# Performance work log

Measured on AMD Instinct MI355X. Metric: run time of the kernel, lower is better.

Reference implementation:

```python
import jax, jax.numpy as jnp
import numpy as np

B, DIM, H, W = 2, 384, 256, 256
HID = DIM * 1          # ffn_expansion_factor = 1 (required for source code to be consistent)
P = 8                  # patch_size


def setup_inputs() -> dict:
    key = jax.random.key(0)
    k0, k1, k2, k3, k4 = jax.random.split(key, 5)
    x = jax.random.normal(k0, (B, DIM, H, W), jnp.float32)
    # learned spectral filter: (hidden, P, P//2+1), real-valued, multiplies rfft2 coeffs
    fft_filter = jax.random.normal(k1, (HID, P, P // 2 + 1), jnp.float32)
    # project_in: 1x1 conv dim->hidden, weight (out,in)
    w_in = jax.random.normal(k2, (HID, DIM), jnp.float32) * (1.0 / np.sqrt(DIM))
    # depthwise 3x3 conv, groups=channels, weight (C,1,3,3)
    w_dw = jax.random.normal(k3, (HID, 1, 3, 3), jnp.float32) * (1.0 / 3.0)
    # project_out: 1x1 conv hidden//2 -> dim
    w_out = jax.random.normal(k4, (DIM, HID // 2), jnp.float32) * (1.0 / np.sqrt(HID // 2))
    return {"x": x, "fft_filter": fft_filter, "w_in": w_in, "w_dw": w_dw, "w_out": w_out}


def reference(x, fft_filter, w_in, w_dw, w_out):
    b, c, h, w = x.shape
    hid = w_in.shape[0]
    hb, wb = h // P, w // P
    # project_in (1x1 conv == channel GEMM)
    t = jnp.einsum('bchw,oc->bohw', x, w_in)
    # patchify into 8x8 blocks and apply per-patch 2D real FFT spectral filter.
    # reshape b c (hb p1) (wb p2) -> b c hb p1 wb p2; FFT over axes (3,5).
    tp = t.reshape(b, hid, hb, P, wb, P)
    tf = jnp.fft.rfft2(tp, axes=(3, 5))                 # (b,hid,hb,P,wb,P//2+1) complex
    tf = tf * fft_filter[None, :, None, :, None, :]
    tp = jnp.fft.irfft2(tf, s=(P, P), axes=(3, 5))
    t = tp.reshape(b, hid, h, w)
    # depthwise 3x3 conv, stride 1, padding 1
    t = jax.lax.conv_general_dilated(
        t, w_dw, window_strides=(1, 1), padding='SAME',
        feature_group_count=hid,
        dimension_numbers=('NCHW', 'OIHW', 'NCHW'))
    # gated GELU (exact erf gelu, matching torch F.gelu default)
    x1, x2 = t[:, : hid // 2], t[:, hid // 2:]
    g = jax.nn.gelu(x1, approximate=False) * x2
    # project_out (1x1 conv)
    return jnp.einsum('bchw,oc->bohw', g, w_out)
```

## Files before the change

kernel.cpp:

```cpp
#include <hip/hip_runtime.h>
#include <hip/hip_bf16.h>
#include <math.h>

#define BB 2
#define DIM 384
#define HID 384
#define HW 65536

typedef short s16x8 __attribute__((ext_vector_type(8)));
typedef short s16x4 __attribute__((ext_vector_type(4)));
typedef __bf16 bf16x8 __attribute__((ext_vector_type(8)));
typedef float f32x4 __attribute__((ext_vector_type(4)));

__device__ inline short f2b(float f) {
    __hip_bfloat16 h = __float2bfloat16(f);
    return __builtin_bit_cast(short, h);
}
__device__ inline float b2f(short s) {
    return __bfloat162float(__builtin_bit_cast(__hip_bfloat16, s));
}

__device__ inline void gl_lds16(const short* g, short* l) {
    __builtin_amdgcn_global_load_lds(
        (const __attribute__((address_space(1))) unsigned int*)g,
        (__attribute__((address_space(3))) unsigned int*)l, 16, 0, 0);
}

__global__ void k_precompute(const float* __restrict__ F, float* __restrict__ K) {
    int c = blockIdx.x;
    int t = threadIdx.x;
    int a = t >> 3, b = t & 7;
    const float ctab[8] = {1.f, 0.70710678118654752f, 0.f, -0.70710678118654752f,
                           -1.f, -0.70710678118654752f, 0.f, 0.70710678118654752f};
    const float* Fc = F + c * 40;
    float acc = 0.f;
#pragma unroll
    for (int up = 0; up < 8; ++up) {
#pragma unroll
        for (int vp = 0; vp < 5; ++vp) {
            float wv = (vp == 0 || vp == 4) ? 1.f : 2.f;
            int k = (a * up + b * vp) & 7;
            acc += wv * Fc[up * 5 + vp] * ctab[k];
        }
    }
    K[c * 64 + t] = acc * (1.f / 64.f);
}

__global__ void k_cvtw(const float* __restrict__ in, short* __restrict__ out, int n) {
    int i = blockIdx.x * 256 + threadIdx.x;
    if (i < n) out[i] = f2b(in[i]);
}

__global__ __launch_bounds__(256) void k_cvtx(const float* __restrict__ X, short* __restrict__ Xt) {
    int hw0 = blockIdx.x * 64, c0 = blockIdx.y * 64, b = blockIdx.z;
    __shared__ __align__(16) short S[64 * 64];
    int t = threadIdx.x;
    const float* Xb = X + ((size_t)(b * DIM) << 16);
    short* Xtb = Xt + (size_t)b * HW * DIM;
#pragma unroll
    for (int p = 0; p < 2; ++p) {
        int row = p * 32 + (t >> 3), sb = t & 7;
        const float* src = &Xb[((size_t)(c0 + row) << 16) + hw0 + sb * 8];
        float4 a = *(const float4*)src;
        float4 bq = *(const float4*)(src + 4);
        s16x8 v;
        v[0] = f2b(a.x);  v[1] = f2b(a.y);  v[2] = f2b(a.z);  v[3] = f2b(a.w);
        v[4] = f2b(bq.x); v[5] = f2b(bq.y); v[6] = f2b(bq.z); v[7] = f2b(bq.w);
        *(s16x8*)&S[row * 64 + ((sb ^ (row >> 3)) << 3)] = v;
    }
    __syncthreads();
#pragma unroll
    for (int p = 0; p < 2; ++p) {
        int row = p * 32 + (t >> 3), ch = t & 7;
        s16x8 v;
#pragma unroll
        for (int j = 0; j < 8; ++j)
            v[j] = S[(ch * 8 + j) * 64 + (row ^ (ch << 3))];
        *(s16x8*)&Xtb[(size_t)(hw0 + row) * DIM + c0 + ch * 8] = v;
    }
}

__global__ __launch_bounds__(256) void k_gemm1_patch(const short* __restrict__ A,
                                                     const short* __restrict__ Bt,
                                                     short* __restrict__ E) {
    __shared__ __align__(16) short SH[17408];
    short* As = SH;
    short* Bs = SH + 4096;
    int d = blockIdx.x;
    int wg = (d & 7) * 192 + (d >> 3);
    int m0 = (wg % 3) * 128;
    int tx = wg / 3;
    int h0 = (tx >> 4) * 8;
    int w0 = (tx & 15) * 16;
    int b  = blockIdx.z;
    const short* Bz = Bt + (size_t)b * HW * DIM;
    int tid = threadIdx.x;
    int lane = tid & 63, w = tid >> 6;
    int wr = w >> 1, wc = w & 1;
    int lm = lane & 15, quad = lane >> 4;

    f32x4 acc[4][4];
#pragma unroll
    for (int i = 0; i < 4; ++i)
#pragma unroll
        for (int j = 0; j < 4; ++j) acc[i][j] = 0.f;

    int srow = tid >> 2, sseg = tid & 3;
    int pu = srow >> 3, pv = srow & 7;
    int p1 = ((h0 + pu) << 8) + w0 + pv;
    int p2 = p1 + 8;
    for (int k0 = 0; k0 < DIM; k0 += 32) {
        gl_lds16(A + (size_t)(m0 + srow) * DIM + k0 + sseg * 8, As + tid * 8);
        gl_lds16(A + (size_t)(m0 + 64 + srow) * DIM + k0 + sseg * 8, As + (tid + 256) * 8);
        gl_lds16(Bz + (size_t)p1 * DIM + k0 + sseg * 8, Bs + tid * 8);
        gl_lds16(Bz + (size_t)p2 * DIM + k0 + sseg * 8, Bs + (tid + 256) * 8);
        __syncthreads();
        bf16x8 af[4], bfr[4];
#pragma unroll
        for (int i = 0; i < 4; ++i)
            af[i] = __builtin_bit_cast(bf16x8, *(const s16x8*)&As[(wr * 64 + i * 16 + lm) * 32 + quad * 8]);
#pragma unroll
        for (int j = 0; j < 4; ++j)
            bfr[j] = __builtin_bit_cast(bf16x8, *(const s16x8*)&Bs[(wc * 64 + j * 16 + lm) * 32 + quad * 8]);
#pragma unroll
        for (int i = 0; i < 4; ++i)
#pragma unroll
            for (int j = 0; j < 4; ++j)
                acc[i][j] = __builtin_amdgcn_mfma_f32_16x16x32_bf16(af[i], bfr[j], acc[i][j], 0, 0, 0);
        __syncthreads();
    }
#pragma unroll
    for (int i = 0; i < 4; ++i)
#pragma unroll
        for (int j = 0; j < 4; ++j)
#pragma unroll
            for (int r = 0; r < 4; ++r)
                SH[(wr * 64 + i * 16 + quad * 4 + r) * 136 + wc * 64 + j * 16 + lm] =
                    f2b(acc[i][j][r]);
    __syncthreads();
#pragma unroll
    for (int kq = 0; kq < 8; ++kq) {
        int idx = kq * 256 + tid;
        int row = idx >> 4, seg = idx & 15;
        s16x8 vv = *(const s16x8*)&SH[row * 136 + seg * 8];
        *(s16x8*)&E[(((size_t)(b * HID + m0 + row)) << 16) + tx * 128 + seg * 8] = vv;
    }
}

__global__ __launch_bounds__(256) void k_circ(const short* __restrict__ E,
                                              const float* __restrict__ Kt,
                                              short* __restrict__ T) {
    __shared__ __align__(16) short SH[4096 + 8704];
    short* Ms = SH;
    short* Bs = SH + 4096;
    short* Cs = SH + 4096;
    int pt = blockIdx.x;
    int c  = blockIdx.y;
    int b  = blockIdx.z;
    int tid = threadIdx.x;
    int lane = tid & 63, wn = tid >> 6;
    int lm = lane & 15, quad = lane >> 4;

    const float* Kc = Kt + c * 64;
#pragma unroll
    for (int e = 0; e < 16; ++e) {
        int idx = tid * 16 + e;
        int uv = idx >> 6, k = idx & 63;
        int a = ((k >> 3) - (uv >> 3)) & 7;
        int bb = ((k & 7) - (uv & 7)) & 7;
        Ms[uv * 64 + ((((k >> 3) ^ (uv & 7))) << 3) + (k & 7)] = f2b(Kc[a * 8 + bb]);
    }
    const short* Eblk = E + (((size_t)(b * HID + c)) << 16) + pt * 8192;
#pragma unroll
    for (int ps = 0; ps < 4; ++ps)
        gl_lds16(Eblk + ps * 2048 + (tid >> 3) * 64 + (((tid & 7) ^ ((tid >> 3) & 7)) << 3),
                 Bs + ps * 2048 + tid * 8);
    __syncthreads();

    f32x4 acc[4][2];
#pragma unroll
    for (int i = 0; i < 4; ++i) { acc[i][0] = 0.f; acc[i][1] = 0.f; }
#pragma unroll
    for (int ks = 0; ks < 2; ++ks) {
        bf16x8 af[4], bfr[2];
#pragma unroll
        for (int i = 0; i < 4; ++i)
            af[i] = __builtin_bit_cast(bf16x8,
                *(const s16x8*)&Ms[(i * 16 + lm) * 64 + (((ks * 4 + quad) ^ (lm & 7)) << 3)]);
#pragma unroll
        for (int j = 0; j < 2; ++j)
            bfr[j] = __builtin_bit_cast(bf16x8,
                *(const s16x8*)&Bs[(wn * 32 + j * 16 + lm) * 64 + (((ks * 4 + quad) ^ (lm & 7)) << 3)]);
#pragma unroll
        for (int i = 0; i < 4; ++i)
#pragma unroll
            for (int j = 0; j < 2; ++j)
                acc[i][j] = __builtin_amdgcn_mfma_f32_16x16x32_bf16(af[i], bfr[j], acc[i][j], 0, 0, 0);
    }
    __syncthreads();
#pragma unroll
    for (int i = 0; i < 4; ++i)
#pragma unroll
        for (int j = 0; j < 2; ++j)
#pragma unroll
            for (int r = 0; r < 4; ++r)
                Cs[(i * 16 + quad * 4 + r) * 136 + wn * 32 + j * 16 + lm] = f2b(acc[i][j][r]);
    __syncthreads();
    short* Tc = T + (((size_t)(b * HID + c)) << 16);
#pragma unroll
    for (int kq = 0; kq < 4; ++kq) {
        int idx = kq * 256 + tid;
        int u = idx >> 7, pl = idx & 127;
        int pid = pt * 128 + pl;
        s16x8 ov;
#pragma unroll
        for (int v = 0; v < 8; ++v) ov[v] = Cs[(u * 8 + v) * 136 + pl];
        *(s16x8*)&Tc[(size_t)((((pid >> 5) * 8 + u) << 8) + ((pid & 31) << 3))] = ov;
    }
}

__global__ __launch_bounds__(256) void k_dwgt(const short* __restrict__ Y,
                                              const float* __restrict__ Wdw,
                                              short* __restrict__ Gt) {
    int bz = blockIdx.z;
    int b  = bz / 24;
    int cg = bz % 24;
    int c0 = cg * 8;
    int h0 = blockIdx.y * 16, w0 = blockIdx.x * 64;
    __shared__ __align__(16) short S[16][18][80];
    __shared__ float sw[16][9];
    int tid = threadIdx.x;
    if (tid < 144) {
        int p = tid / 9, j = tid % 9;
        int ch = (p < 8) ? (c0 + p) : (c0 + p - 8 + 192);
        sw[p][j] = Wdw[ch * 9 + j];
    }
    for (int t = tid; t < 2880; t += 256) {
        int v = t % 10, r = (t / 10) % 18, p = t / 180;
        int gh = h0 + r - 1;
        int gw = w0 + v * 8 - 8;
        int ch = (p < 8) ? (c0 + p) : (c0 + p - 8 + 192);
        s16x8 val = {0, 0, 0, 0, 0, 0, 0, 0};
        if (gh >= 0 && gh < 256 && gw >= 0 && gw <= 248)
            val = *(const s16x8*)&Y[((size_t)(b * HID + ch) << 16) + (gh << 8) + gw];
        *(s16x8*)&S[p][r][v * 8] = val;
    }
    __syncthreads();
    s16x8 ov[4];
#pragma unroll
    for (int it = 0; it < 4; ++it) {
        int idx = it * 256 + tid;
        int p = idx >> 7, run = idx & 127;
        int r = run >> 3, c8 = (run & 7) * 8;
        float z1[8], z2[8];
#pragma unroll
        for (int k = 0; k < 8; ++k) { z1[k] = 0.f; z2[k] = 0.f; }
#pragma unroll
        for (int i = 0; i < 3; ++i) {
            {
                s16x4 wv[4];
#pragma unroll
                for (int q = 0; q < 4; ++q) wv[q] = *(const s16x4*)&S[p][r + i][c8 + 4 + q * 4];
                float fv[10];
#pragma unroll
                for (int q = 0; q < 10; ++q) fv[q] = b2f(wv[(q + 3) >> 2][(q + 3) & 3]);
#pragma unroll
                for (int j = 0; j < 3; ++j) {
                    float wgt = sw[p][i * 3 + j];
#pragma unroll
                    for (int k = 0; k < 8; ++k) z1[k] += fv[k + j] * wgt;
                }
            }
            {
                s16x4 wv[4];
#pragma unroll
                for (int q = 0; q < 4; ++q) wv[q] = *(const s16x4*)&S[p + 8][r + i][c8 + 4 + q * 4];
                float fv[10];
#pragma unroll
                for (int q = 0; q < 10; ++q) fv[q] = b2f(wv[(q + 3) >> 2][(q + 3) & 3]);
#pragma unroll
                for (int j = 0; j < 3; ++j) {
                    float wgt = sw[p + 8][i * 3 + j];
#pragma unroll
                    for (int k = 0; k < 8; ++k) z2[k] += fv[k + j] * wgt;
                }
            }
        }
#pragma unroll
        for (int k = 0; k < 8; ++k) {
            float g = 0.5f * z1[k] * (1.f + erff(z1[k] * 0.70710678118654752f));
            ov[it][k] = f2b(g * z2[k]);
        }
    }
    __syncthreads();
    short* Ob = (short*)S;
#pragma unroll
    for (int it = 0; it < 4; ++it) {
        int idx = it * 256 + tid;
        int p = idx >> 7, run = idx & 127;
        int pos = (run >> 3) * 64 + (run & 7) * 8;
#pragma unroll
        for (int k = 0; k < 8; ++k)
            Ob[(pos + k) * 9 + p] = ov[it][k];
    }
    __syncthreads();
    short* Gb = Gt + (((size_t)(b * 24 + cg)) << 16) * 8;
#pragma unroll
    for (int it = 0; it < 4; ++it) {
        int pos = it * 256 + tid;
        int r = pos >> 6, cl = pos & 63;
        s16x8 v;
#pragma unroll
        for (int k = 0; k < 8; ++k) v[k] = Ob[pos * 9 + k];
        *(s16x8*)&Gb[(size_t)(((h0 + r) << 8) + w0 + cl) * 8] = v;
    }
}

__global__ __launch_bounds__(256) void k_gemm_bf16(const short* __restrict__ A,
                                                   const short* __restrict__ Bt,
                                                   float* __restrict__ C,
                                                   int N, int K) {
    __shared__ __align__(16) short As[128 * 32];
    __shared__ __align__(16) short Bs[128 * 32];
    const short* Bz = Bt + (size_t)blockIdx.z * (size_t)N * K;
    float* Cz = C + (size_t)blockIdx.z * (size_t)384 * N;
    int d = blockIdx.x;
    int wg = (d & 7) * 192 + (d >> 3);
    int m0 = (wg % 3) * 128;
    int n0 = (wg / 3) * 128;
    int tid = threadIdx.x;
    int lane = tid & 63, w = tid >> 6;
    int wr = w >> 1, wc = w & 1;
    int lm = lane & 15, quad = lane >> 4;

    f32x4 acc[4][4];
#pragma unroll
    for (int i = 0; i < 4; ++i)
#pragma unroll
        for (int j = 0; j < 4; ++j) acc[i][j] = 0.f;

    int srow = tid >> 2, sseg = tid & 3;
    for (int k0 = 0; k0 < K; k0 += 32) {
        gl_lds16(A + (size_t)(m0 + srow) * K + k0 + sseg * 8, As + tid * 8);
        gl_lds16(A + (size_t)(m0 + 64 + srow) * K + k0 + sseg * 8, As + (tid + 256) * 8);
        gl_lds16(Bz + ((size_t)((k0 >> 3) + sseg) * HW + n0 + srow) * 8, Bs + tid * 8);
        gl_lds16(Bz + ((size_t)((k0 >> 3) + sseg) * HW + n0 + 64 + srow) * 8, Bs + (tid + 256) * 8);
        __syncthreads();
        bf16x8 af[4], bfr[4];
#pragma unroll
        for (int i = 0; i < 4; ++i)
            af[i] = __builtin_bit_cast(bf16x8, *(const s16x8*)&As[(wr * 64 + i * 16 + lm) * 32 + quad * 8]);
#pragma unroll
        for (int j = 0; j < 4; ++j)
            bfr[j] = __builtin_bit_cast(bf16x8, *(const s16x8*)&Bs[(wc * 64 + j * 16 + lm) * 32 + quad * 8]);
#pragma unroll
        for (int i = 0; i < 4; ++i)
#pragma unroll
            for (int j = 0; j < 4; ++j)
                acc[i][j] = __builtin_amdgcn_mfma_f32_16x16x32_bf16(af[i], bfr[j], acc[i][j], 0, 0, 0);
        __syncthreads();
    }
#pragma unroll
    for (int i = 0; i < 4; ++i) {
        int r0 = m0 + wr * 64 + i * 16 + quad * 4;
#pragma unroll
        for (int j = 0; j < 4; ++j) {
            int cidx = n0 + wc * 64 + j * 16 + lm;
#pragma unroll
            for (int r = 0; r < 4; ++r)
                Cz[(size_t)(r0 + r) * N + cidx] = acc[i][j][r];
        }
    }
}

extern "C" void kernel_launch(void* const* d_in, const int* in_sizes, int n_in,
                              void* d_out, int out_size, void* d_ws, size_t ws_size,
                              hipStream_t stream) {
    const float* x     = (const float*)d_in[0];
    const float* ff    = (const float*)d_in[1];
    const float* w_in  = (const float*)d_in[2];
    const float* w_dw  = (const float*)d_in[3];
    const float* w_out = (const float*)d_in[4];
    float* out = (float*)d_out;

    char* ws = (char*)d_ws;
    float* Kbuf = (float*)ws;
    short* wbin = (short*)(ws + 98304);
    short* wbout = (short*)(ws + 393216);
    short* bufA = (short*)(ws + 540672);
    short* bufB = (short*)(ws + 540672 + (size_t)100663296);
    short* Gt = bufB;

    k_precompute<<<384, 64, 0, stream>>>(ff, Kbuf);
    k_cvtw<<<(DIM * DIM + 255) / 256, 256, 0, stream>>>(w_in, wbin, DIM * DIM);
    k_cvtw<<<(DIM * 192 + 255) / 256, 256, 0, stream>>>(w_out, wbout, DIM * 192);
    k_cvtx<<<dim3(HW / 64, DIM / 64, BB), 256, 0, stream>>>(x, bufA);

    k_gemm1_patch<<<dim3(1536, 1, BB), 256, 0, stream>>>(wbin, bufA, bufB);

    k_circ<<<dim3(8, 384, BB), 256, 0, stream>>>(bufB, Kbuf, bufA);

    k_dwgt<<<dim3(4, 16, BB * 24), 256, 0, stream>>>(bufA, w_dw, Gt);

    k_gemm_bf16<<<dim3(1536, 1, BB), 256, 0, stream>>>(wbout, Gt, out, HW, 192);
}
```

Before: 585.9 us.

## Fuse per-patch spectral filter into project_in GEMM via Hartley-transform diagonalization

Replaces the separate circulant-matrix kernel with an in-register epilogue of the first GEMM. Each 8x8 patch tile goes through a 2D Hartley (cas) transform, a per-channel diagonal multiply and a second cas transform, all as small MFMA GEMMs on LDS-resident data. This removes a full bf16 round trip of the hidden activation through global memory and one kernel launch. In exchange the GEMM kernel uses more LDS and registers and adds extra bf16 rounding steps.

```diff
diff --git a/kernel.cpp b/kernel.cpp
--- a/kernel.cpp
+++ b/kernel.cpp
@@ -26,24 +26,26 @@
         (__attribute__((address_space(3))) unsigned int*)l, 16, 0, 0);
 }
 
-__global__ void k_precompute(const float* __restrict__ F, float* __restrict__ K) {
-    int c = blockIdx.x;
-    int t = threadIdx.x;
-    int a = t >> 3, b = t & 7;
-    const float ctab[8] = {1.f, 0.70710678118654752f, 0.f, -0.70710678118654752f,
-                           -1.f, -0.70710678118654752f, 0.f, 0.70710678118654752f};
-    const float* Fc = F + c * 40;
-    float acc = 0.f;
-#pragma unroll
-    for (int up = 0; up < 8; ++up) {
-#pragma unroll
-        for (int vp = 0; vp < 5; ++vp) {
-            float wv = (vp == 0 || vp == 4) ? 1.f : 2.f;
-            int k = (a * up + b * vp) & 7;
-            acc += wv * Fc[up * 5 + vp] * ctab[k];
-        }
-    }
-    K[c * 64 + t] = acc * (1.f / 64.f);
+__global__ void k_prepR(short* __restrict__ Rb) {
+    int idx = blockIdx.x * 256 + threadIdx.x;
+    int j = idx >> 6, k = idx & 63;
+    const float cas[8] = {1.f, 1.41421356237f, 1.f, 0.f, -1.f, -1.41421356237f, -1.f, 0.f};
+    int t = ((j >> 3) * (k >> 3) + (j & 7) * (k & 7)) & 7;
+    Rb[idx] = f2b(cas[t]);
+}
+
+__global__ void k_prepD(const float* __restrict__ F, float* __restrict__ Dt) {
+    int idx = blockIdx.x * 256 + threadIdx.x;
+    int c = idx >> 6, j = idx & 63;
+    int a = j >> 3, q = j & 7;
+    float d;
+    if (q >= 1 && q <= 3)
+        d = F[c * 40 + a * 5 + q];
+    else if (q >= 5)
+        d = F[c * 40 + ((8 - a) & 7) * 5 + (8 - q)];
+    else
+        d = 0.5f * (F[c * 40 + a * 5 + q] + F[c * 40 + ((8 - a) & 7) * 5 + q]);
+    Dt[j * 384 + c] = d * (1.f / 64.f);
 }
 
 __global__ void k_cvtw(const float* __restrict__ in, short* __restrict__ out, int n) {
@@ -80,12 +82,15 @@
     }
 }
 
-__global__ __launch_bounds__(256) void k_gemm1_patch(const short* __restrict__ A,
-                                                     const short* __restrict__ Bt,
-                                                     short* __restrict__ E) {
-    __shared__ __align__(16) short SH[17408];
+__global__ __launch_bounds__(256) void k_gemm1c(const short* __restrict__ A,
+                                                const short* __restrict__ Bt,
+                                                const short* __restrict__ Rb,
+                                                const float* __restrict__ Dt,
+                                                short* __restrict__ T) {
+    __shared__ __align__(16) short SH[17408 + 4096];
     short* As = SH;
     short* Bs = SH + 4096;
+    short* Rs = SH + 17408;
     int d = blockIdx.x;
     int wg = (d & 7) * 192 + (d >> 3);
     int m0 = (wg % 3) * 128;
@@ -99,6 +104,14 @@
     int wr = w >> 1, wc = w & 1;
     int lm = lane & 15, quad = lane >> 4;
 
+    {
+        int j0 = tid >> 3, kb0 = tid & 7;
+        gl_lds16(Rb + j0 * 64 + ((kb0 ^ (j0 & 7)) << 3), Rs + tid * 8);
+        int t2 = tid + 256;
+        int j1 = t2 >> 3, kb1 = t2 & 7;
+        gl_lds16(Rb + j1 * 64 + ((kb1 ^ (j1 & 7)) << 3), Rs + t2 * 8);
+    }
+
     f32x4 acc[4][4];
 #pragma unroll
     for (int i = 0; i < 4; ++i)
@@ -138,84 +151,87 @@
                 SH[(wr * 64 + i * 16 + quad * 4 + r) * 136 + wc * 64 + j * 16 + lm] =
                     f2b(acc[i][j][r]);
     __syncthreads();
+
+    f32x4 acc2[4][4];
+#pragma unroll
+    for (int i = 0; i < 4; ++i)
+#pragma unroll
+        for (int j = 0; j < 4; ++j) acc2[i][j] = 0.f;
+#pragma unroll
+    for (int ks = 0; ks < 2; ++ks) {
+        bf16x8 af[4], bfr[4];
+#pragma unroll
+        for (int i = 0; i < 4; ++i)
+            af[i] = __builtin_bit_cast(bf16x8,
+                *(const s16x8*)&SH[(wr * 64 + i * 16 + lm) * 136 + wc * 64 + ks * 32 + quad * 8]);
+#pragma unroll
+        for (int jf = 0; jf < 4; ++jf)
+            bfr[jf] = __builtin_bit_cast(bf16x8,
+                *(const s16x8*)&Rs[(jf * 16 + lm) * 64 + (((ks * 4 + quad) ^ (lm & 7)) << 3)]);
+#pragma unroll
+        for (int i = 0; i < 4; ++i)
+#pragma unroll
+            for (int jf = 0; jf < 4; ++jf)
+                acc2[i][jf] = __builtin_amdgcn_mfma_f32_16x16x32_bf16(af[i], bfr[jf], acc2[i][jf], 0, 0, 0);
+    }
+#pragma unroll
+    for (int i = 0; i < 4; ++i)
+#pragma unroll
+        for (int jf = 0; jf < 4; ++jf) {
+            int j = jf * 16 + lm;
+            float4 dv = *(const float4*)&Dt[j * 384 + m0 + wr * 64 + i * 16 + quad * 4];
+            acc2[i][jf][0] *= dv.x; acc2[i][jf][1] *= dv.y;
+            acc2[i][jf][2] *= dv.z; acc2[i][jf][3] *= dv.w;
+        }
+    __syncthreads();
+#pragma unroll
+    for (int i = 0; i < 4; ++i)
+#pragma unroll
+        for (int jf = 0; jf < 4; ++jf)
+#pragma unroll
+            for (int r = 0; r < 4; ++r)
+                SH[(wr * 64 + i * 16 + quad * 4 + r) * 136 + wc * 64 + jf * 16 + lm] =
+                    f2b(acc2[i][jf][r]);
+    __syncthreads();
+
+    f32x4 acc3[4][4];
+#pragma unroll
+    for (int i = 0; i < 4; ++i)
+#pragma unroll
+        for (int j = 0; j < 4; ++j) acc3[i][j] = 0.f;
+#pragma unroll
+    for (int ks = 0; ks < 2; ++ks) {
+        bf16x8 af[4], bfr[4];
+#pragma unroll
+        for (int i = 0; i < 4; ++i)
+            af[i] = __builtin_bit_cast(bf16x8,
+                *(const s16x8*)&SH[(wr * 64 + i * 16 + lm) * 136 + wc * 64 + ks * 32 + quad * 8]);
+#pragma unroll
+        for (int uf = 0; uf < 4; ++uf)
+            bfr[uf] = __builtin_bit_cast(bf16x8,
+                *(const s16x8*)&Rs[(uf * 16 + lm) * 64 + (((ks * 4 + quad) ^ (lm & 7)) << 3)]);
+#pragma unroll
+        for (int i = 0; i < 4; ++i)
+#pragma unroll
+            for (int uf = 0; uf < 4; ++uf)
+                acc3[i][uf] = __builtin_amdgcn_mfma_f32_16x16x32_bf16(af[i], bfr[uf], acc3[i][uf], 0, 0, 0);
+    }
+    __syncthreads();
+#pragma unroll
+    for (int i = 0; i < 4; ++i)
+#pragma unroll
+        for (int uf = 0; uf < 4; ++uf)
+#pragma unroll
+            for (int r = 0; r < 4; ++r)
+                SH[(wr * 64 + i * 16 + quad * 4 + r) * 136 + wc * 64 + uf * 16 + lm] =
+                    f2b(acc3[i][uf][r]);
+    __syncthreads();
 #pragma unroll
     for (int kq = 0; kq < 8; ++kq) {
         int idx = kq * 256 + tid;
-        int row = idx >> 4, seg = idx & 15;
-        s16x8 vv = *(const s16x8*)&SH[row * 136 + seg * 8];
-        *(s16x8*)&E[(((size_t)(b * HID + m0 + row)) << 16) + tx * 128 + seg * 8] = vv;
-    }
-}
-
-__global__ __launch_bounds__(256) void k_circ(const short* __restrict__ E,
-                                              const float* __restrict__ Kt,
-                                              short* __restrict__ T) {
-    __shared__ __align__(16) short SH[4096 + 8704];
-    short* Ms = SH;
-    short* Bs = SH + 4096;
-    short* Cs = SH + 4096;
-    int pt = blockIdx.x;
-    int c  = blockIdx.y;
-    int b  = blockIdx.z;
-    int tid = threadIdx.x;
-    int lane = tid & 63, wn = tid >> 6;
-    int lm = lane & 15, quad = lane >> 4;
-
-    const float* Kc = Kt + c * 64;
-#pragma unroll
-    for (int e = 0; e < 16; ++e) {
-        int idx = tid * 16 + e;
-        int uv = idx >> 6, k = idx & 63;
-        int a = ((k >> 3) - (uv >> 3)) & 7;
-        int bb = ((k & 7) - (uv & 7)) & 7;
-        Ms[uv * 64 + ((((k >> 3) ^ (uv & 7))) << 3) + (k & 7)] = f2b(Kc[a * 8 + bb]);
-    }
-    const short* Eblk = E + (((size_t)(b * HID + c)) << 16) + pt * 8192;
-#pragma unroll
-    for (int ps = 0; ps < 4; ++ps)
-        gl_lds16(Eblk + ps * 2048 + (tid >> 3) * 64 + (((tid & 7) ^ ((tid >> 3) & 7)) << 3),
-                 Bs + ps * 2048 + tid * 8);
-    __syncthreads();
-
-    f32x4 acc[4][2];
-#pragma unroll
-    for (int i = 0; i < 4; ++i) { acc[i][0] = 0.f; acc[i][1] = 0.f; }
-#pragma unroll
-    for (int ks = 0; ks < 2; ++ks) {
-        bf16x8 af[4], bfr[2];
-#pragma unroll
-        for (int i = 0; i < 4; ++i)
-            af[i] = __builtin_bit_cast(bf16x8,
-                *(const s16x8*)&Ms[(i * 16 + lm) * 64 + (((ks * 4 + quad) ^ (lm & 7)) << 3)]);
-#pragma unroll
-        for (int j = 0; j < 2; ++j)
-            bfr[j] = __builtin_bit_cast(bf16x8,
-                *(const s16x8*)&Bs[(wn * 32 + j * 16 + lm) * 64 + (((ks * 4 + quad) ^ (lm & 7)) << 3)]);
-#pragma unroll
-        for (int i = 0; i < 4; ++i)
-#pragma unroll
-            for (int j = 0; j < 2; ++j)
-                acc[i][j] = __builtin_amdgcn_mfma_f32_16x16x32_bf16(af[i], bfr[j], acc[i][j], 0, 0, 0);
-    }
-    __syncthreads();
-#pragma unroll
-    for (int i = 0; i < 4; ++i)
-#pragma unroll
-        for (int j = 0; j < 2; ++j)
-#pragma unroll
-            for (int r = 0; r < 4; ++r)
-                Cs[(i * 16 + quad * 4 + r) * 136 + wn * 32 + j * 16 + lm] = f2b(acc[i][j][r]);
-    __syncthreads();
-    short* Tc = T + (((size_t)(b * HID + c)) << 16);
-#pragma unroll
-    for (int kq = 0; kq < 4; ++kq) {
-        int idx = kq * 256 + tid;
-        int u = idx >> 7, pl = idx & 127;
-        int pid = pt * 128 + pl;
-        s16x8 ov;
-#pragma unroll
-        for (int v = 0; v < 8; ++v) ov[v] = Cs[(u * 8 + v) * 136 + pl];
-        *(s16x8*)&Tc[(size_t)((((pid >> 5) * 8 + u) << 8) + ((pid & 31) << 3))] = ov;
+        int pat = idx & 1, ch = (idx >> 1) & 127, u = idx >> 8;
+        s16x8 vv = *(const s16x8*)&SH[ch * 136 + pat * 64 + u * 8];
+        *(s16x8*)&T[(((size_t)(b * HID + m0 + ch)) << 16) + ((h0 + u) << 8) + w0 + pat * 8] = vv;
     }
 }
 
@@ -384,23 +400,23 @@
     float* out = (float*)d_out;
 
     char* ws = (char*)d_ws;
-    float* Kbuf = (float*)ws;
+    float* Dt   = (float*)ws;
     short* wbin = (short*)(ws + 98304);
     short* wbout = (short*)(ws + 393216);
-    short* bufA = (short*)(ws + 540672);
-    short* bufB = (short*)(ws + 540672 + (size_t)100663296);
-    short* Gt = bufB;
-
-    k_precompute<<<384, 64, 0, stream>>>(ff, Kbuf);
+    short* Rbuf = (short*)(ws + 540672);
+    short* bufA = (short*)(ws + 548864);
+    short* bufB = (short*)(ws + 548864 + (size_t)100663296);
+    short* Gt = bufA;
+
+    k_prepR<<<16, 256, 0, stream>>>(Rbuf);
+    k_prepD<<<96, 256, 0, stream>>>(ff, Dt);
     k_cvtw<<<(DIM * DIM + 255) / 256, 256, 0, stream>>>(w_in, wbin, DIM * DIM);
     k_cvtw<<<(DIM * 192 + 255) / 256, 256, 0, stream>>>(w_out, wbout, DIM * 192);
     k_cvtx<<<dim3(HW / 64, DIM / 64, BB), 256, 0, stream>>>(x, bufA);
 
-    k_gemm1_patch<<<dim3(1536, 1, BB), 256, 0, stream>>>(wbin, bufA, bufB);
-
-    k_circ<<<dim3(8, 384, BB), 256, 0, stream>>>(bufB, Kbuf, bufA);
-
-    k_dwgt<<<dim3(4, 16, BB * 24), 256, 0, stream>>>(bufA, w_dw, Gt);
+    k_gemm1c<<<dim3(1536, 1, BB), 256, 0, stream>>>(wbin, bufA, Rbuf, Dt, bufB);
+
+    k_dwgt<<<dim3(4, 16, BB * 24), 256, 0, stream>>>(bufB, w_dw, Gt);
 
     k_gemm_bf16<<<dim3(1536, 1, BB), 256, 0, stream>>>(wbout, Gt, out, HW, 192);
 }
```

New measurement: 599.6 us. 1.02x slower.
